# Performance work log

Measured on AMD Instinct MI355X. Metric: run time of the kernel, lower is better.

The kernel has to match this reference:

```python
import jax, jax.numpy as jnp
import numpy as np

N_NODES = 100000
N_EDGES = 1600000
IN_FEATS = 128
HIDDEN = 150
NUM_OUT = 128


def setup_inputs() -> dict:
    key = jax.random.key(0)
    ks = jax.random.split(key, 9)
    x = jax.random.normal(ks[0], (N_NODES, IN_FEATS), dtype=jnp.float32)
    src = jax.random.randint(ks[1], (N_EDGES,), 0, N_NODES, dtype=jnp.int32)
    dst = jax.random.randint(ks[2], (N_EDGES,), 0, N_NODES, dtype=jnp.int32)
    def lin(k, fan_in, fan_out):
        bound = 1.0 / np.sqrt(fan_in)
        return jax.random.uniform(k, (fan_in, fan_out), jnp.float32, -bound, bound)
    W_self1 = lin(ks[3], IN_FEATS, HIDDEN)
    W_neigh1 = lin(ks[4], IN_FEATS, HIDDEN)
    b1 = jnp.zeros((HIDDEN,), jnp.float32)
    W_self2 = lin(ks[5], HIDDEN, NUM_OUT)
    W_neigh2 = lin(ks[6], HIDDEN, NUM_OUT)
    b2 = jnp.zeros((NUM_OUT,), jnp.float32)
    return {"x": x, "src": src, "dst": dst,
            "W_self1": W_self1, "W_neigh1": W_neigh1, "b1": b1,
            "W_self2": W_self2, "W_neigh2": W_neigh2, "b2": b2}


def _mean_agg(h, src, dst, deg_inv):
    # segment-mean of source features onto destination nodes; isolated nodes -> 0
    summed = jax.ops.segment_sum(h[src], dst, num_segments=N_NODES)
    return summed * deg_inv[:, None]


def _sage_conv(h, src, dst, deg_inv, W_self, W_neigh, b):
    h_neigh = _mean_agg(h, src, dst, deg_inv)
    return h @ W_self + h_neigh @ W_neigh + b


def reference(x, src, dst, W_self1, W_neigh1, b1, W_self2, W_neigh2, b2):
    deg = jax.ops.segment_sum(jnp.ones((src.shape[0],), x.dtype), dst,
                              num_segments=N_NODES)
    deg_inv = jnp.where(deg > 0, 1.0 / jnp.maximum(deg, 1.0), 0.0)
    h = _sage_conv(x, src, dst, deg_inv, W_self1, W_neigh1, b1)
    h = jax.nn.relu(h)
    h = _sage_conv(h, src, dst, deg_inv, W_self2, W_neigh2, b2)
    return h
```

## Files before the change

### kernel.cpp

```cpp
#include <hip/hip_runtime.h>

#define NN 100000
#define NE 1600000
#define INF 128
#define HID 150
#define NOUT 128

#define NBK 196
#define WGS 400
#define EPW 4000
#define CNTL (NBK * WGS)
#define CAP2 10240

typedef __attribute__((ext_vector_type(8))) short bf16x8;
typedef __attribute__((ext_vector_type(8))) unsigned short u16x8;
typedef __attribute__((ext_vector_type(4))) float f32x4;
typedef __attribute__((ext_vector_type(2))) float f32x2;

__device__ inline unsigned short f2bf(float f) {
    unsigned int u = __float_as_uint(f);
    u += 0x7fffu + ((u >> 16) & 1u);
    return (unsigned short)(u >> 16);
}
__device__ inline float bflo(unsigned int t) { return __uint_as_float(t << 16); }
__device__ inline float bfhi(unsigned int t) { return __uint_as_float(t & 0xffff0000u); }


__global__ __launch_bounds__(256) void sort1(const int* __restrict__ src,
                                             const int* __restrict__ dst,
                                             unsigned int* __restrict__ chunkw,
                                             int* __restrict__ cntm) {
    __shared__ int hist[NBK];
    __shared__ int off[NBK];
    __shared__ int s[256];
    __shared__ unsigned int buf[EPW];
    int w = blockIdx.x, tid = threadIdx.x;
    int e0 = w * EPW;
    for (int i = tid; i < NBK; i += 256) hist[i] = 0;
    __syncthreads();
    for (int i = tid; i < EPW; i += 256) atomicAdd(&hist[dst[e0 + i] >> 9], 1);
    __syncthreads();
    int v = (tid < NBK) ? hist[tid] : 0;
    s[tid] = v;
    __syncthreads();
    for (int o = 1; o < 256; o <<= 1) {
        int t = (tid >= o) ? s[tid - o] : 0;
        __syncthreads();
        s[tid] += t;
        __syncthreads();
    }
    if (tid < NBK) {
        off[tid] = s[tid] - v;
        cntm[tid * WGS + w] = v;
    }
    __syncthreads();
    for (int i = tid; i < EPW; i += 256) {
        int d = dst[e0 + i];
        int b = d >> 9;
        int p = atomicAdd(&off[b], 1);
        buf[p] = (unsigned int)src[e0 + i] | ((unsigned int)(d & 511) << 17);
    }
    __syncthreads();
    for (int i = tid; i < EPW; i += 256) chunkw[e0 + i] = buf[i];
}

__global__ void scanA(const int* __restrict__ in, int* __restrict__ excl,
                      int* __restrict__ blk_sums, int L) {
    __shared__ int s[256];
    int i = blockIdx.x * 256 + threadIdx.x;
    int d = (i < L) ? in[i] : 0;
    s[threadIdx.x] = d;
    __syncthreads();
    for (int o = 1; o < 256; o <<= 1) {
        int t = (threadIdx.x >= o) ? s[threadIdx.x - o] : 0;
        __syncthreads();
        s[threadIdx.x] += t;
        __syncthreads();
    }
    int incl = s[threadIdx.x];
    if (i < L) excl[i] = incl - d;
    if (threadIdx.x == 255) blk_sums[blockIdx.x] = incl;
}

__global__ void scanB(int* __restrict__ blk_sums, int nb) {
    __shared__ int s[512];
    int t = threadIdx.x;
    int v = (t < nb) ? blk_sums[t] : 0;
    s[t] = v;
    __syncthreads();
    for (int o = 1; o < 512; o <<= 1) {
        int u = (t >= o) ? s[t - o] : 0;
        __syncthreads();
        s[t] += u;
        __syncthreads();
    }
    if (t < nb) blk_sums[t] = s[t] - v;
}

__global__ void scanC(int* __restrict__ excl, const int* __restrict__ blk_sums, int L) {
    int i = blockIdx.x * 256 + threadIdx.x;
    if (i < L) excl[i] += blk_sums[blockIdx.x];
}

__global__ __launch_bounds__(256) void sort3(const unsigned int* __restrict__ chunkw,
                                             const int* __restrict__ cntm,
                                             const int* __restrict__ offm,
                                             unsigned int* __restrict__ bmaj) {
    __shared__ int excl[NBK + 1];
    __shared__ int dbase[NBK];
    __shared__ int s[256];
    int w = blockIdx.x, tid = threadIdx.x;
    int v = (tid < NBK) ? cntm[tid * WGS + w] : 0;
    if (tid < NBK) dbase[tid] = offm[tid * WGS + w];
    s[tid] = v;
    __syncthreads();
    for (int o = 1; o < 256; o <<= 1) {
        int t = (tid >= o) ? s[tid - o] : 0;
        __syncthreads();
        s[tid] += t;
        __syncthreads();
    }
    if (tid < NBK) excl[tid] = s[tid] - v;
    if (tid == 0) excl[NBK] = EPW;
    __syncthreads();
    int e0 = w * EPW;
    for (int i = tid; i < EPW; i += 256) {
        int lo = 0, hi = NBK;
        while (hi - lo > 1) {
            int mid = (lo + hi) >> 1;
            if (excl[mid] <= i) lo = mid; else hi = mid;
        }
        bmaj[dbase[lo] + (i - excl[lo])] = chunkw[e0 + i];
    }
}

__global__ __launch_bounds__(256) void buildcsr(const unsigned int* __restrict__ bmaj,
                                                const int* __restrict__ offm,
                                                int* __restrict__ csr_ptr,
                                                float* __restrict__ deg_inv,
                                                int* __restrict__ csr_src) {
    __shared__ int cnt[512];
    __shared__ int excl[512];
    __shared__ int off[512];
    __shared__ int s[256];
    __shared__ int span[CAP2];
    int b = blockIdx.x, tid = threadIdx.x;
    int base = offm[b * WGS];
    int nxt = (b == NBK - 1) ? NE : offm[(b + 1) * WGS];
    int n = nxt - base;
    if (n > CAP2) n = CAP2;
    for (int i = tid; i < 512; i += 256) cnt[i] = 0;
    __syncthreads();
    for (int i = tid; i < n; i += 256) atomicAdd(&cnt[bmaj[base + i] >> 17], 1);
    __syncthreads();
    int a0 = cnt[2 * tid], a1 = cnt[2 * tid + 1];
    int ps = a0 + a1;
    s[tid] = ps;
    __syncthreads();
    for (int o = 1; o < 256; o <<= 1) {
        int t = (tid >= o) ? s[tid - o] : 0;
        __syncthreads();
        s[tid] += t;
        __syncthreads();
    }
    int ex = s[tid] - ps;
    excl[2 * tid] = ex;
    excl[2 * tid + 1] = ex + a0;
    off[2 * tid] = ex;
    off[2 * tid + 1] = ex + a0;
    __syncthreads();
    for (int l = tid; l < 512; l += 256) {
        int g = b * 512 + l;
        if (g < NN) {
            csr_ptr[g] = base + excl[l];
            int d = cnt[l];
            deg_inv[g] = d > 0 ? 1.0f / (float)d : 0.0f;
        }
    }
    if (b == NBK - 1 && tid == 0) csr_ptr[NN] = NE;
    for (int i = tid; i < n; i += 256) {
        unsigned int wd = bmaj[base + i];
        int l = wd >> 17;
        int p = atomicAdd(&off[l], 1);
        span[p] = (int)(wd & 0x1FFFFu);
    }
    __syncthreads();
    for (int i = tid; i < n; i += 256) csr_src[base + i] = span[i];
}


__global__ void cast_bf16(const float* __restrict__ in, unsigned short* __restrict__ outb,
                          int n8) {
    int i = blockIdx.x * 256 + threadIdx.x;
    if (i >= n8) return;
    const f32x4* p = (const f32x4*)in;
    f32x4 v0 = __builtin_nontemporal_load(&p[(size_t)i * 2]);
    f32x4 v1 = __builtin_nontemporal_load(&p[(size_t)i * 2 + 1]);
    u16x8 o = {f2bf(v0[0]), f2bf(v0[1]), f2bf(v0[2]), f2bf(v0[3]),
               f2bf(v1[0]), f2bf(v1[1]), f2bf(v1[2]), f2bf(v1[3])};
    ((u16x8*)outb)[i] = o;
}

__global__ void pack_weights(const float* __restrict__ Ws1, const float* __restrict__ Wn1,
                             const float* __restrict__ b1,
                             const float* __restrict__ Ws2, const float* __restrict__ Wn2,
                             unsigned short* __restrict__ W1t, unsigned short* __restrict__ W2t,
                             float* __restrict__ b1p) {
    int id = blockIdx.x * 256 + threadIdx.x;
    if (id < 160 * 256) {
        int n = id >> 8, k = id & 255;
        float v = 0.f;
        if (n < HID) v = (k < 128) ? Ws1[k * HID + n] : Wn1[(k - 128) * HID + n];
        W1t[id] = f2bf(v);
    } else if (id < 160 * 256 + 256 * 160) {
        int id2 = id - 160 * 256;
        int n = id2 / 160, k = id2 - n * 160;
        float v = 0.f;
        if (k < HID) v = (n < 128) ? Ws2[k * 128 + n] : Wn2[k * 128 + (n - 128)];
        W2t[id2] = f2bf(v);
    } else if (id < 160 * 256 + 256 * 160 + 160) {
        int n = id - (160 * 256 + 256 * 160);
        b1p[n] = (n < HID) ? b1[n] : 0.f;
    }
}


#define AGG_ACC(t)                              \
    accA += (f32x2){bflo(t.x), bfhi(t.x)};      \
    accB += (f32x2){bflo(t.y), bfhi(t.y)};      \
    accC += (f32x2){bflo(t.z), bfhi(t.z)};      \
    accD += (f32x2){bflo(t.w), bfhi(t.w)};

#define AGG_BODY(FTBL)                                                 \
    int e = start;                                                     \
    for (; e + 16 <= end; e += 16) {                                   \
        int s0 = csr_src[e + rg];                                      \
        int s1 = csr_src[e + 4 + rg];                                  \
        int s2 = csr_src[e + 8 + rg];                                  \
        int s3 = csr_src[e + 12 + rg];                                 \
        uint4 t0 = FTBL[(size_t)s0 * 16 + ch];                         \
        uint4 t1 = FTBL[(size_t)s1 * 16 + ch];                         \
        uint4 t2 = FTBL[(size_t)s2 * 16 + ch];                         \
        uint4 t3 = FTBL[(size_t)s3 * 16 + ch];                         \
        AGG_ACC(t0);                                                   \
        AGG_ACC(t1);                                                   \
        AGG_ACC(t2);                                                   \
        AGG_ACC(t3);                                                   \
    }                                                                  \
    if (e + 8 <= end) {                                                \
        int s0 = csr_src[e + rg];                                      \
        int s1 = csr_src[e + 4 + rg];                                  \
        uint4 t0 = FTBL[(size_t)s0 * 16 + ch];                         \
        uint4 t1 = FTBL[(size_t)s1 * 16 + ch];                         \
        AGG_ACC(t0);                                                   \
        AGG_ACC(t1);                                                   \
        e += 8;                                                        \
    }                                                                  \
    if (e + 4 <= end) {                                                \
        int s0 = csr_src[e + rg];                                      \
        uint4 t0 = FTBL[(size_t)s0 * 16 + ch];                         \
        AGG_ACC(t0);                                                   \
        e += 4;                                                        \
    }                                                                  \
    int rem = end - e;                                                 \
    if (rem > 0) {                                                     \
        int s0 = csr_src[(rg < rem) ? (e + rg) : e];                   \
        uint4 t = FTBL[(size_t)s0 * 16 + ch];                          \
        float wt = (rg < rem) ? 1.f : 0.f;                             \
        f32x2 w2 = {wt, wt};                                           \
        accA += w2 * (f32x2){bflo(t.x), bfhi(t.x)};                    \
        accB += w2 * (f32x2){bflo(t.y), bfhi(t.y)};                    \
        accC += w2 * (f32x2){bflo(t.z), bfhi(t.z)};                    \
        accD += w2 * (f32x2){bflo(t.w), bfhi(t.w)};                    \
    }                                                                  \
    float acc0 = accA[0], acc1 = accA[1];                              \
    float acc2 = accB[0], acc3 = accB[1];                              \
    float acc4 = accC[0], acc5 = accC[1];                              \
    float acc6 = accD[0], acc7 = accD[1];                              \
    acc0 += __shfl_xor(acc0, 32); acc1 += __shfl_xor(acc1, 32);        \
    acc2 += __shfl_xor(acc2, 32); acc3 += __shfl_xor(acc3, 32);        \
    acc4 += __shfl_xor(acc4, 32); acc5 += __shfl_xor(acc5, 32);        \
    acc6 += __shfl_xor(acc6, 32); acc7 += __shfl_xor(acc7, 32);        \
    acc0 += __shfl_xor(acc0, 16); acc1 += __shfl_xor(acc1, 16);        \
    acc2 += __shfl_xor(acc2, 16); acc3 += __shfl_xor(acc3, 16);        \
    acc4 += __shfl_xor(acc4, 16); acc5 += __shfl_xor(acc5, 16);        \
    acc6 += __shfl_xor(acc6, 16); acc7 += __shfl_xor(acc7, 16);

__global__ __launch_bounds__(256) void agg_mean_q(
    const unsigned short* __restrict__ featb, const int* __restrict__ csr_ptr,
    const float* __restrict__ deg_inv, const int* __restrict__ csr_src,
    unsigned short* __restrict__ outb) {
    int wid = threadIdx.x >> 6;
    int lane = threadIdx.x & 63;
    int v = blockIdx.x * 4 + wid;
    int start = csr_ptr[v], end = csr_ptr[v + 1];
    int rg = lane >> 4, ch = lane & 15;
    const uint4* f4 = (const uint4*)featb;
    f32x2 accA = {0.f, 0.f}, accB = {0.f, 0.f};
    f32x2 accC = {0.f, 0.f}, accD = {0.f, 0.f};
    AGG_BODY(f4);
    if (lane < 16) {
        float di = deg_inv[v];
        u16x8 o = {f2bf(acc0 * di), f2bf(acc1 * di), f2bf(acc2 * di), f2bf(acc3 * di),
                   f2bf(acc4 * di), f2bf(acc5 * di), f2bf(acc6 * di), f2bf(acc7 * di)};
        ((u16x8*)outb)[(size_t)v * 16 + ch] = o;
    }
}

__global__ __launch_bounds__(256) void agg_add_q(
    const unsigned short* __restrict__ zb, const int* __restrict__ csr_ptr,
    const float* __restrict__ deg_inv, const int* __restrict__ csr_src,
    float* __restrict__ out) {
    int wid = threadIdx.x >> 6;
    int lane = threadIdx.x & 63;
    int v = blockIdx.x * 4 + wid;
    int start = csr_ptr[v], end = csr_ptr[v + 1];
    int rg = lane >> 4, ch = lane & 15;
    const uint4* f4 = (const uint4*)zb;
    f32x2 accA = {0.f, 0.f}, accB = {0.f, 0.f};
    f32x2 accC = {0.f, 0.f}, accD = {0.f, 0.f};
    AGG_BODY(f4);
    if (lane < 16) {
        float di = deg_inv[v];
        f32x4* o4 = (f32x4*)out;
        size_t base = (size_t)v * 32 + ch * 2;
        f32x4 c0 = __builtin_nontemporal_load(&o4[base]);
        f32x4 c1 = __builtin_nontemporal_load(&o4[base + 1]);
        c0[0] += acc0 * di; c0[1] += acc1 * di; c0[2] += acc2 * di; c0[3] += acc3 * di;
        c1[0] += acc4 * di; c1[1] += acc5 * di; c1[2] += acc6 * di; c1[3] += acc7 * di;
        __builtin_nontemporal_store(c0, &o4[base]);
        __builtin_nontemporal_store(c1, &o4[base + 1]);
    }
}


__global__ __launch_bounds__(256, 4) void gemm1_mfma(
    const unsigned short* __restrict__ xb, const unsigned short* __restrict__ aggb,
    const unsigned short* __restrict__ W1t, const float* __restrict__ b1p,
    unsigned short* __restrict__ h1b) {
    __shared__ __align__(16) unsigned short A_lds[64][40];
    __shared__ __align__(16) unsigned short B_lds[160][40];
    int tid = threadIdx.x;
    int m0 = blockIdx.x * 64;
    int w = tid >> 6, lane = tid & 63;
    int lrow = lane & 15, quad = lane >> 4;
    int wr = (w & 1) * 32;
    int wc = (w >> 1) * 80;
    f32x4 acc[2][5];
    #pragma unroll
    for (int r = 0; r < 2; r++)
        #pragma unroll
        for (int c = 0; c < 5; c++) acc[r][c] = (f32x4){0.f, 0.f, 0.f, 0.f};

    for (int k0 = 0; k0 < 256; k0 += 32) {
        __syncthreads();
        {
            int row = tid >> 2, ch = tid & 3;
            int gm = m0 + row, gk = k0 + ch * 8;
            u16x8 val = {0, 0, 0, 0, 0, 0, 0, 0};
            if (gm < NN) {
                const unsigned short* sp = (gk < 128)
                    ? (xb + (size_t)gm * 128 + gk)
                    : (aggb + (size_t)gm * 128 + (gk - 128));
                val = *(const u16x8*)sp;
            }
            *(u16x8*)&A_lds[row][ch * 8] = val;
        }
        #pragma unroll
        for (int i = 0; i < 3; i++) {
            int idx = tid + i * 256;
            if (idx < 640) {
                int n = idx >> 2, ch = idx & 3;
                u16x8 val = *(const u16x8*)(W1t + (size_t)n * 256 + k0 + ch * 8);
                *(u16x8*)&B_lds[n][ch * 8] = val;
            }
        }
        __syncthreads();
        bf16x8 a[2], b[5];
        #pragma unroll
        for (int r = 0; r < 2; r++)
            a[r] = *(const bf16x8*)&A_lds[wr + r * 16 + lrow][quad * 8];
        #pragma unroll
        for (int c = 0; c < 5; c++)
            b[c] = *(const bf16x8*)&B_lds[wc + c * 16 + lrow][quad * 8];
        #pragma unroll
        for (int r = 0; r < 2; r++)
            #pragma unroll
            for (int c = 0; c < 5; c++)
                acc[r][c] = __builtin_amdgcn_mfma_f32_16x16x32_bf16(a[r], b[c], acc[r][c], 0, 0, 0);
    }
    #pragma unroll
    for (int r = 0; r < 2; r++) {
        #pragma unroll
        for (int rr = 0; rr < 4; rr++) {
            int gm = m0 + wr + r * 16 + quad * 4 + rr;
            if (gm < NN) {
                #pragma unroll
                for (int c = 0; c < 5; c++) {
                    int gn = wc + c * 16 + lrow;
                    float val = acc[r][c][rr] + b1p[gn];
                    val = val > 0.f ? val : 0.f;
                    h1b[(size_t)gm * 160 + gn] = f2bf(val);
                }
            }
        }
    }
}

__global__ __launch_bounds__(256, 4) void gemm2_mfma(
    const unsigned short* __restrict__ h1b, const unsigned short* __restrict__ W2t,
    const float* __restrict__ b2, float* __restrict__ out,
    unsigned short* __restrict__ zb) {
    __shared__ __align__(16) unsigned short A_lds[64][40];
    __shared__ __align__(16) unsigned short B_lds[128][40];
    int tid = threadIdx.x;
    int m0 = blockIdx.x * 64;
    int n0 = blockIdx.y * 128;
    int w = tid >> 6, lane = tid & 63;
    int lrow = lane & 15, quad = lane >> 4;
    int wr = (w & 1) * 32;
    int wc = (w >> 1) * 64;
    f32x4 acc[2][4];
    #pragma unroll
    for (int r = 0; r < 2; r++)
        #pragma unroll
        for (int c = 0; c < 4; c++) acc[r][c] = (f32x4){0.f, 0.f, 0.f, 0.f};

    for (int k0 = 0; k0 < 160; k0 += 32) {
        __syncthreads();
        {
            int row = tid >> 2, ch = tid & 3;
            int gm = m0 + row;
            u16x8 val = {0, 0, 0, 0, 0, 0, 0, 0};
            if (gm < NN) val = *(const u16x8*)(h1b + (size_t)gm * 160 + k0 + ch * 8);
            *(u16x8*)&A_lds[row][ch * 8] = val;
        }
        #pragma unroll
        for (int i = 0; i < 2; i++) {
            int idx = tid + i * 256;
            int n = idx >> 2, ch = idx & 3;
            u16x8 val = *(const u16x8*)(W2t + (size_t)(n0 + n) * 160 + k0 + ch * 8);
            *(u16x8*)&B_lds[n][ch * 8] = val;
        }
        __syncthreads();
        bf16x8 a[2], b[4];
        #pragma unroll
        for (int r = 0; r < 2; r++)
            a[r] = *(const bf16x8*)&A_lds[wr + r * 16 + lrow][quad * 8];
        #pragma unroll
        for (int c = 0; c < 4; c++)
            b[c] = *(const bf16x8*)&B_lds[wc + c * 16 + lrow][quad * 8];
        #pragma unroll
        for (int r = 0; r < 2; r++)
            #pragma unroll
            for (int c = 0; c < 4; c++)
                acc[r][c] = __builtin_amdgcn_mfma_f32_16x16x32_bf16(a[r], b[c], acc[r][c], 0, 0, 0);
    }
    #pragma unroll
    for (int r = 0; r < 2; r++) {
        #pragma unroll
        for (int rr = 0; rr < 4; rr++) {
            int gm = m0 + wr + r * 16 + quad * 4 + rr;
            if (gm < NN) {
                #pragma unroll
                for (int c = 0; c < 4; c++) {
                    int gn = wc + c * 16 + lrow;
                    float val = acc[r][c][rr];
                    if (n0 == 0) {
                        out[(size_t)gm * 128 + gn] = val + b2[gn];
                    } else {
                        zb[(size_t)gm * 128 + gn] = f2bf(val);
                    }
                }
            }
        }
    }
}


extern "C" void kernel_launch(void* const* d_in, const int* in_sizes, int n_in,
                              void* d_out, int out_size, void* d_ws, size_t ws_size,
                              hipStream_t stream) {
    const float* x   = (const float*)d_in[0];
    const int* src   = (const int*)d_in[1];
    const int* dst   = (const int*)d_in[2];
    const float* Ws1 = (const float*)d_in[3];
    const float* Wn1 = (const float*)d_in[4];
    const float* b1  = (const float*)d_in[5];
    const float* Ws2 = (const float*)d_in[6];
    const float* Wn2 = (const float*)d_in[7];
    const float* b2  = (const float*)d_in[8];
    float* out = (float*)d_out;

    char* p = (char*)d_ws;
    auto carve = [&](size_t bytes) {
        void* r = (void*)p;
        p += (bytes + 255) & ~(size_t)255;
        return r;
    };
    int*   csr_ptr  = (int*)carve((size_t)(NN + 1) * 4);
    float* deg_inv  = (float*)carve((size_t)NN * 4);
    int*   csr_src  = (int*)carve((size_t)NE * 4);
    int*   cntm     = (int*)carve((size_t)CNTL * 4);
    int*   offm     = (int*)carve((size_t)CNTL * 4);
    int*   blk2     = (int*)carve(512 * 4);
    unsigned short* xb   = (unsigned short*)carve((size_t)NN * 128 * 2);
    unsigned short* aggb = (unsigned short*)carve((size_t)NN * 128 * 2);
    unsigned short* zb   = (unsigned short*)carve((size_t)NN * 128 * 2);
    unsigned short* W1t  = (unsigned short*)carve(160 * 256 * 2);
    unsigned short* W2t  = (unsigned short*)carve(256 * 160 * 2);
    float* b1p           = (float*)carve(160 * 4);
    unsigned short* h1b  = (unsigned short*)carve((size_t)NN * 160 * 2);
    unsigned int* chunkw = (unsigned int*)h1b;
    unsigned int* bmaj   = (unsigned int*)((char*)h1b + (size_t)NE * 4);

    sort1<<<WGS, 256, 0, stream>>>(src, dst, chunkw, cntm);
    const int SB = (CNTL + 255) / 256;
    scanA<<<SB, 256, 0, stream>>>(cntm, offm, blk2, CNTL);
    scanB<<<1, 512, 0, stream>>>(blk2, SB);
    scanC<<<SB, 256, 0, stream>>>(offm, blk2, CNTL);
    sort3<<<WGS, 256, 0, stream>>>(chunkw, cntm, offm, bmaj);
    buildcsr<<<NBK, 256, 0, stream>>>(bmaj, offm, csr_ptr, deg_inv, csr_src);

    cast_bf16<<<(NN * 128 / 8 + 255) / 256, 256, 0, stream>>>(x, xb, NN * 128 / 8);
    pack_weights<<<(160 * 256 + 256 * 160 + 160 + 255) / 256, 256, 0, stream>>>(
        Ws1, Wn1, b1, Ws2, Wn2, W1t, W2t, b1p);

    agg_mean_q<<<NN / 4, 256, 0, stream>>>(xb, csr_ptr, deg_inv, csr_src, aggb);
    gemm1_mfma<<<dim3((NN + 63) / 64, 1), 256, 0, stream>>>(xb, aggb, W1t, b1p, h1b);

    gemm2_mfma<<<dim3((NN + 63) / 64, 2), 256, 0, stream>>>(h1b, W2t, b2, out, zb);
    agg_add_q<<<NN / 4, 256, 0, stream>>>(zb, csr_ptr, deg_inv, csr_src, out);

    (void)in_sizes; (void)n_in; (void)out_size; (void)ws_size;
}
```

Measured before the change: 364.4 us.

## Fuse layer-1 mean aggregation into the first GEMM via shared memory

The separate layer-1 aggregation kernel is removed. Each GEMM block now gathers and averages neighbour features for its 64 rows into an LDS buffer, then reads the neighbour half of the A operand from LDS instead of from a global bf16 buffer. This saves one launch and a full global write and read of the aggregated features. In exchange, each block serialises gather work over 16 nodes per wave before the MFMA loop, and the extra 17KB of LDS may lower occupancy, so latency hiding of the random gathers may get worse.

```diff
diff --git a/kernel.cpp b/kernel.cpp
--- a/kernel.cpp
+++ b/kernel.cpp
@@ -286,27 +286,6 @@
     acc4 += __shfl_xor(acc4, 16); acc5 += __shfl_xor(acc5, 16);        \
     acc6 += __shfl_xor(acc6, 16); acc7 += __shfl_xor(acc7, 16);
 
-__global__ __launch_bounds__(256) void agg_mean_q(
-    const unsigned short* __restrict__ featb, const int* __restrict__ csr_ptr,
-    const float* __restrict__ deg_inv, const int* __restrict__ csr_src,
-    unsigned short* __restrict__ outb) {
-    int wid = threadIdx.x >> 6;
-    int lane = threadIdx.x & 63;
-    int v = blockIdx.x * 4 + wid;
-    int start = csr_ptr[v], end = csr_ptr[v + 1];
-    int rg = lane >> 4, ch = lane & 15;
-    const uint4* f4 = (const uint4*)featb;
-    f32x2 accA = {0.f, 0.f}, accB = {0.f, 0.f};
-    f32x2 accC = {0.f, 0.f}, accD = {0.f, 0.f};
-    AGG_BODY(f4);
-    if (lane < 16) {
-        float di = deg_inv[v];
-        u16x8 o = {f2bf(acc0 * di), f2bf(acc1 * di), f2bf(acc2 * di), f2bf(acc3 * di),
-                   f2bf(acc4 * di), f2bf(acc5 * di), f2bf(acc6 * di), f2bf(acc7 * di)};
-        ((u16x8*)outb)[(size_t)v * 16 + ch] = o;
-    }
-}
-
 __global__ __launch_bounds__(256) void agg_add_q(
     const unsigned short* __restrict__ zb, const int* __restrict__ csr_ptr,
     const float* __restrict__ deg_inv, const int* __restrict__ csr_src,
@@ -334,15 +313,39 @@
 }
 
 
-__global__ __launch_bounds__(256, 4) void gemm1_mfma(
-    const unsigned short* __restrict__ xb, const unsigned short* __restrict__ aggb,
+__global__ __launch_bounds__(256, 4) void fused1(
+    const unsigned short* __restrict__ xb, const int* __restrict__ csr_ptr,
+    const float* __restrict__ deg_inv, const int* __restrict__ csr_src,
     const unsigned short* __restrict__ W1t, const float* __restrict__ b1p,
     unsigned short* __restrict__ h1b) {
     __shared__ __align__(16) unsigned short A_lds[64][40];
     __shared__ __align__(16) unsigned short B_lds[160][40];
+    __shared__ __align__(16) unsigned short A2[64][136];
     int tid = threadIdx.x;
     int m0 = blockIdx.x * 64;
     int w = tid >> 6, lane = tid & 63;
+
+    {
+        int rg = lane >> 4, ch = lane & 15;
+        const uint4* f4 = (const uint4*)xb;
+        #pragma unroll 1
+        for (int i = 0; i < 16; i++) {
+            int v = m0 + w * 16 + i;
+            f32x2 accA = {0.f, 0.f}, accB = {0.f, 0.f};
+            f32x2 accC = {0.f, 0.f}, accD = {0.f, 0.f};
+            int start = 0, end = 0;
+            if (v < NN) { start = csr_ptr[v]; end = csr_ptr[v + 1]; }
+            AGG_BODY(f4);
+            if (lane < 16) {
+                float di = (v < NN) ? deg_inv[v] : 0.f;
+                u16x8 o = {f2bf(acc0 * di), f2bf(acc1 * di), f2bf(acc2 * di), f2bf(acc3 * di),
+                           f2bf(acc4 * di), f2bf(acc5 * di), f2bf(acc6 * di), f2bf(acc7 * di)};
+                *(u16x8*)&A2[w * 16 + i][ch * 8] = o;
+            }
+        }
+    }
+    __syncthreads();
+
     int lrow = lane & 15, quad = lane >> 4;
     int wr = (w & 1) * 32;
     int wc = (w >> 1) * 80;
@@ -356,13 +359,12 @@
         __syncthreads();
         {
             int row = tid >> 2, ch = tid & 3;
-            int gm = m0 + row, gk = k0 + ch * 8;
             u16x8 val = {0, 0, 0, 0, 0, 0, 0, 0};
-            if (gm < NN) {
-                const unsigned short* sp = (gk < 128)
-                    ? (xb + (size_t)gm * 128 + gk)
-                    : (aggb + (size_t)gm * 128 + (gk - 128));
-                val = *(const u16x8*)sp;
+            if (k0 < 128) {
+                int gm = m0 + row, gk = k0 + ch * 8;
+                if (gm < NN) val = *(const u16x8*)(xb + (size_t)gm * 128 + gk);
+            } else {
+                val = *(const u16x8*)&A2[row][(k0 - 128) + ch * 8];
             }
             *(u16x8*)&A_lds[row][ch * 8] = val;
         }
@@ -406,6 +408,7 @@
         }
     }
 }
+
 
 __global__ __launch_bounds__(256, 4) void gemm2_mfma(
     const unsigned short* __restrict__ h1b, const unsigned short* __restrict__ W2t,
@@ -505,7 +508,6 @@
     int*   offm     = (int*)carve((size_t)CNTL * 4);
     int*   blk2     = (int*)carve(512 * 4);
     unsigned short* xb   = (unsigned short*)carve((size_t)NN * 128 * 2);
-    unsigned short* aggb = (unsigned short*)carve((size_t)NN * 128 * 2);
     unsigned short* zb   = (unsigned short*)carve((size_t)NN * 128 * 2);
     unsigned short* W1t  = (unsigned short*)carve(160 * 256 * 2);
     unsigned short* W2t  = (unsigned short*)carve(256 * 160 * 2);
@@ -526,8 +528,8 @@
     pack_weights<<<(160 * 256 + 256 * 160 + 160 + 255) / 256, 256, 0, stream>>>(
         Ws1, Wn1, b1, Ws2, Wn2, W1t, W2t, b1p);
 
-    agg_mean_q<<<NN / 4, 256, 0, stream>>>(xb, csr_ptr, deg_inv, csr_src, aggb);
-    gemm1_mfma<<<dim3((NN + 63) / 64, 1), 256, 0, stream>>>(xb, aggb, W1t, b1p, h1b);
+    fused1<<<dim3((NN + 63) / 64, 1), 256, 0, stream>>>(
+        xb, csr_ptr, deg_inv, csr_src, W1t, b1p, h1b);
 
     gemm2_mfma<<<dim3((NN + 63) / 64, 2), 256, 0, stream>>>(h1b, W2t, b2, out, zb);
     agg_add_q<<<NN / 4, 256, 0, stream>>>(zb, csr_ptr, deg_inv, csr_src, out);
```

Result: slower. 388.7 us (+6.7%).

## Fuse bucket scatter into CSR build by reading per-chunk segments directly

Applied to the files above, without the earlier changes.

Drops the separate sort3 pass that scattered chunk-local sorted edges into a bucket-major array. sort1 now also records each chunk's per-bucket start offset, and the CSR builder walks the 400 chunk segments for its bucket straight out of chunkw. This removes a kernel launch and a full write and read of the intermediate edge array. In exchange, each thread serially loops over short, scattered segments, with poor coalescing and uneven work because only 256 threads cover 400 segments.

```diff
diff --git a/kernel.cpp b/kernel.cpp
--- a/kernel.cpp
+++ b/kernel.cpp
@@ -29,7 +29,8 @@
 __global__ __launch_bounds__(256) void sort1(const int* __restrict__ src,
                                              const int* __restrict__ dst,
                                              unsigned int* __restrict__ chunkw,
-                                             int* __restrict__ cntm) {
+                                             int* __restrict__ cntm,
+                                             int* __restrict__ segsta) {
     __shared__ int hist[NBK];
     __shared__ int off[NBK];
     __shared__ int s[256];
@@ -50,8 +51,10 @@
         __syncthreads();
     }
     if (tid < NBK) {
-        off[tid] = s[tid] - v;
+        int ex = s[tid] - v;
+        off[tid] = ex;
         cntm[tid * WGS + w] = v;
+        segsta[tid * WGS + w] = ex;
     }
     __syncthreads();
     for (int i = tid; i < EPW; i += 256) {
@@ -102,43 +105,13 @@
     if (i < L) excl[i] += blk_sums[blockIdx.x];
 }
 
-__global__ __launch_bounds__(256) void sort3(const unsigned int* __restrict__ chunkw,
-                                             const int* __restrict__ cntm,
-                                             const int* __restrict__ offm,
-                                             unsigned int* __restrict__ bmaj) {
-    __shared__ int excl[NBK + 1];
-    __shared__ int dbase[NBK];
-    __shared__ int s[256];
-    int w = blockIdx.x, tid = threadIdx.x;
-    int v = (tid < NBK) ? cntm[tid * WGS + w] : 0;
-    if (tid < NBK) dbase[tid] = offm[tid * WGS + w];
-    s[tid] = v;
-    __syncthreads();
-    for (int o = 1; o < 256; o <<= 1) {
-        int t = (tid >= o) ? s[tid - o] : 0;
-        __syncthreads();
-        s[tid] += t;
-        __syncthreads();
-    }
-    if (tid < NBK) excl[tid] = s[tid] - v;
-    if (tid == 0) excl[NBK] = EPW;
-    __syncthreads();
-    int e0 = w * EPW;
-    for (int i = tid; i < EPW; i += 256) {
-        int lo = 0, hi = NBK;
-        while (hi - lo > 1) {
-            int mid = (lo + hi) >> 1;
-            if (excl[mid] <= i) lo = mid; else hi = mid;
-        }
-        bmaj[dbase[lo] + (i - excl[lo])] = chunkw[e0 + i];
-    }
-}
-
-__global__ __launch_bounds__(256) void buildcsr(const unsigned int* __restrict__ bmaj,
-                                                const int* __restrict__ offm,
-                                                int* __restrict__ csr_ptr,
-                                                float* __restrict__ deg_inv,
-                                                int* __restrict__ csr_src) {
+__global__ __launch_bounds__(256) void buildcsr2(const unsigned int* __restrict__ chunkw,
+                                                 const int* __restrict__ cntm,
+                                                 const int* __restrict__ segsta,
+                                                 const int* __restrict__ offm,
+                                                 int* __restrict__ csr_ptr,
+                                                 float* __restrict__ deg_inv,
+                                                 int* __restrict__ csr_src) {
     __shared__ int cnt[512];
     __shared__ int excl[512];
     __shared__ int off[512];
@@ -151,7 +124,11 @@
     if (n > CAP2) n = CAP2;
     for (int i = tid; i < 512; i += 256) cnt[i] = 0;
     __syncthreads();
-    for (int i = tid; i < n; i += 256) atomicAdd(&cnt[bmaj[base + i] >> 17], 1);
+    for (int sg = tid; sg < WGS; sg += 256) {
+        int c = cntm[b * WGS + sg];
+        int st = sg * EPW + segsta[b * WGS + sg];
+        for (int j = 0; j < c; j++) atomicAdd(&cnt[chunkw[st + j] >> 17], 1);
+    }
     __syncthreads();
     int a0 = cnt[2 * tid], a1 = cnt[2 * tid + 1];
     int ps = a0 + a1;
@@ -178,11 +155,15 @@
         }
     }
     if (b == NBK - 1 && tid == 0) csr_ptr[NN] = NE;
-    for (int i = tid; i < n; i += 256) {
-        unsigned int wd = bmaj[base + i];
-        int l = wd >> 17;
-        int p = atomicAdd(&off[l], 1);
-        span[p] = (int)(wd & 0x1FFFFu);
+    for (int sg = tid; sg < WGS; sg += 256) {
+        int c = cntm[b * WGS + sg];
+        int st = sg * EPW + segsta[b * WGS + sg];
+        for (int j = 0; j < c; j++) {
+            unsigned int wd = chunkw[st + j];
+            int l = wd >> 17;
+            int p = atomicAdd(&off[l], 1);
+            if (p < CAP2) span[p] = (int)(wd & 0x1FFFFu);
+        }
     }
     __syncthreads();
     for (int i = tid; i < n; i += 256) csr_src[base + i] = span[i];
@@ -503,6 +484,7 @@
     int*   csr_src  = (int*)carve((size_t)NE * 4);
     int*   cntm     = (int*)carve((size_t)CNTL * 4);
     int*   offm     = (int*)carve((size_t)CNTL * 4);
+    int*   segsta   = (int*)carve((size_t)CNTL * 4);
     int*   blk2     = (int*)carve(512 * 4);
     unsigned short* xb   = (unsigned short*)carve((size_t)NN * 128 * 2);
     unsigned short* aggb = (unsigned short*)carve((size_t)NN * 128 * 2);
@@ -512,15 +494,14 @@
     float* b1p           = (float*)carve(160 * 4);
     unsigned short* h1b  = (unsigned short*)carve((size_t)NN * 160 * 2);
     unsigned int* chunkw = (unsigned int*)h1b;
-    unsigned int* bmaj   = (unsigned int*)((char*)h1b + (size_t)NE * 4);
-
-    sort1<<<WGS, 256, 0, stream>>>(src, dst, chunkw, cntm);
+
+    sort1<<<WGS, 256, 0, stream>>>(src, dst, chunkw, cntm, segsta);
     const int SB = (CNTL + 255) / 256;
     scanA<<<SB, 256, 0, stream>>>(cntm, offm, blk2, CNTL);
     scanB<<<1, 512, 0, stream>>>(blk2, SB);
     scanC<<<SB, 256, 0, stream>>>(offm, blk2, CNTL);
-    sort3<<<WGS, 256, 0, stream>>>(chunkw, cntm, offm, bmaj);
-    buildcsr<<<NBK, 256, 0, stream>>>(bmaj, offm, csr_ptr, deg_inv, csr_src);
+    buildcsr2<<<NBK, 256, 0, stream>>>(chunkw, cntm, segsta, offm,
+                                       csr_ptr, deg_inv, csr_src);
 
     cast_bf16<<<(NN * 128 / 8 + 255) / 256, 256, 0, stream>>>(x, xb, NN * 128 / 8);
     pack_weights<<<(160 * 256 + 256 * 160 + 160 + 255) / 256, 256, 0, stream>>>(
```

Measured after the change: 355.2 us, median of 2. 1.03x faster.
